# Performance work log

Measured on AMD Instinct MI355X. Metric: run time of the kernel, lower is better.

## Reference

```python
import jax, jax.numpy as jnp
import numpy as np

N_USERS = 50000
N_ITEMS = 100000
N_GROUPS = 20000
D = 128
NNZ_U = 1000000
NNZ_I = 2000000
NNZ_F = 3000000


def setup_inputs() -> dict:
    key = jax.random.key(0)
    ks = jax.random.split(key, 14)
    user_emb = jax.random.normal(ks[0], (N_USERS, D), jnp.float32)
    item_emb = jax.random.normal(ks[1], (N_ITEMS, D), jnp.float32)
    group_emb = jax.random.normal(ks[2], (N_GROUPS, D), jnp.float32)
    # user hypergraph incidence [N_GROUPS, N_USERS] in COO
    u_rows = jax.random.randint(ks[3], (NNZ_U,), 0, N_GROUPS)
    u_cols = jax.random.randint(ks[4], (NNZ_U,), 0, N_USERS)
    u_vals = jax.random.uniform(ks[5], (NNZ_U,), jnp.float32)
    # item hypergraph incidence [N_GROUPS, N_ITEMS] in COO
    i_rows = jax.random.randint(ks[6], (NNZ_I,), 0, N_GROUPS)
    i_cols = jax.random.randint(ks[7], (NNZ_I,), 0, N_ITEMS)
    i_vals = jax.random.uniform(ks[8], (NNZ_I,), jnp.float32)
    # full hypergraph [N_USERS+N_ITEMS, N_GROUPS] in COO
    f_rows = jax.random.randint(ks[9], (NNZ_F,), 0, N_USERS + N_ITEMS)
    f_cols = jax.random.randint(ks[10], (NNZ_F,), 0, N_GROUPS)
    f_vals = jax.random.uniform(ks[11], (NNZ_F,), jnp.float32)
    # nn.Linear(2D, D): weight [D, 2D], bias [D]
    W_agg = jax.random.normal(ks[12], (D, 2 * D), jnp.float32) * 0.05
    b_agg = jnp.zeros((D,), jnp.float32)
    return dict(user_emb=user_emb, item_emb=item_emb, group_emb=group_emb,
                u_rows=u_rows, u_cols=u_cols, u_vals=u_vals,
                i_rows=i_rows, i_cols=i_cols, i_vals=i_vals,
                f_rows=f_rows, f_cols=f_cols, f_vals=f_vals,
                W_agg=W_agg, b_agg=b_agg)


def _spmm(rows, cols, vals, dense, num_rows):
    # sparse[rows, cols]=vals (COO) @ dense -> [num_rows, d]
    return jax.ops.segment_sum(vals[:, None] * dense[cols], rows, num_segments=num_rows)


def reference(user_emb, item_emb, group_emb,
              u_rows, u_cols, u_vals,
              i_rows, i_cols, i_vals,
              f_rows, f_cols, f_vals,
              W_agg, b_agg):
    user_msg = _spmm(u_rows, u_cols, u_vals, user_emb, N_GROUPS)   # [G, D]
    item_msg = _spmm(i_rows, i_cols, i_vals, item_emb, N_GROUPS)   # [G, D]
    msg = jnp.concatenate([user_msg, item_msg], axis=1) @ W_agg.T + b_agg  # [G, D]
    norm_emb = _spmm(f_rows, f_cols, f_vals, msg, N_USERS + N_ITEMS)       # [U+I, D]
    return (norm_emb, msg)
```

## Files before the change

### kernel.cpp

```cpp
#include <hip/hip_runtime.h>
#include <hip/hip_bf16.h>
#include <stdint.h>

#define N_USERS  50000
#define N_ITEMS  100000
#define N_GROUPS 20000
#define DIM      128
#define TWO_DIM  256
#define N_FULL   (N_USERS + N_ITEMS)

#define NBU  625
#define NBI  1250
#define NBF  2344
#define NBT  (NBU + NBI + NBF)
#define CAP  2048

#define TILE_E 32768
#define NT     184
#define NT_PER_XCD 23

__device__ __forceinline__ unsigned bf16_rne(float f)
{
    unsigned u = __float_as_uint(f);
    return (u + 0x7FFFu + ((u >> 16) & 1u)) >> 16;
}
__device__ __forceinline__ unsigned bf16_pack(float a, float b)
{
    return bf16_rne(a) | (bf16_rne(b) << 16);
}

__global__ __launch_bounds__(256) void f32_to_bf16(
    const float4* __restrict__ src, uint2* __restrict__ dst, int n4)
{
    int stride = gridDim.x * 256;
    for (int i = blockIdx.x * 256 + threadIdx.x; i < n4; i += stride) {
        float4 v = src[i];
        dst[i] = make_uint2(bf16_pack(v.x, v.y), bf16_pack(v.z, v.w));
    }
}

__global__ __launch_bounds__(256) void spmm_atomic(
    const int* __restrict__ rows, const int* __restrict__ cols,
    const float* __restrict__ vals, const float* __restrict__ dense,
    float* __restrict__ out, int nnz)
{
    long long t = (long long)blockIdx.x * blockDim.x + threadIdx.x;
    int e    = (int)(t >> 5);
    int lane = (int)(t & 31);
    if (e >= nnz) return;
    int   r = rows[e];
    int   c = cols[e];
    float v = vals[e];
    float4 x = ((const float4*)(dense + (size_t)c * DIM))[lane];
    float* dst = out + (size_t)r * DIM + lane * 4;
    atomicAdd(dst + 0, v * x.x);
    atomicAdd(dst + 1, v * x.y);
    atomicAdd(dst + 2, v * x.z);
    atomicAdd(dst + 3, v * x.w);
}

__device__ __forceinline__ int bucket_of(long long t,
    const int* __restrict__ u_rows, int nnz_u,
    const int* __restrict__ i_rows, int nnz_i,
    const int* __restrict__ f_rows)
{
    if (t < nnz_u)                          return u_rows[t] >> 5;
    else if (t < (long long)nnz_u + nnz_i)  return NBU + (i_rows[t - nnz_u] >> 4);
    else                                    return NBU + NBI + (f_rows[t - nnz_u - nnz_i] >> 6);
}

__global__ __launch_bounds__(512) void hist_tiles(
    const int* __restrict__ u_rows, int nnz_u,
    const int* __restrict__ i_rows, int nnz_i,
    const int* __restrict__ f_rows, int nnz_f,
    unsigned short* __restrict__ M)
{
    __shared__ int h[NBT];
    int tid = threadIdx.x;
    for (int i = tid; i < NBT; i += 512) h[i] = 0;
    __syncthreads();
    int t = (blockIdx.x & 7) * NT_PER_XCD + (blockIdx.x >> 3);
    long long total = (long long)nnz_u + nnz_i + nnz_f;
    long long base  = (long long)t * TILE_E;
    for (int j = tid; j < TILE_E; j += 512) {
        long long e = base + j;
        if (e >= total) break;
        atomicAdd(&h[bucket_of(e, u_rows, nnz_u, i_rows, nnz_i, f_rows)], 1);
    }
    __syncthreads();
    unsigned short* Mrow = M + (size_t)t * NBT;
    for (int i = tid; i < NBT; i += 512) Mrow[i] = (unsigned short)h[i];
}

__global__ __launch_bounds__(64) void tile_prefix(
    unsigned short* __restrict__ M, int* __restrict__ btot)
{
    int b = blockIdx.x * 64 + threadIdx.x;
    if (b >= NBT) return;
    int run = 0;
#pragma unroll 1
    for (int t = 0; t < NT; t += 4) {
        size_t i0 = (size_t)(t + 0) * NBT + b;
        size_t i1 = (size_t)(t + 1) * NBT + b;
        size_t i2 = (size_t)(t + 2) * NBT + b;
        size_t i3 = (size_t)(t + 3) * NBT + b;
        int v0 = M[i0], v1 = M[i1], v2 = M[i2], v3 = M[i3];
        M[i0] = (unsigned short)run; run += v0;
        M[i1] = (unsigned short)run; run += v1;
        M[i2] = (unsigned short)run; run += v2;
        M[i3] = (unsigned short)run; run += v3;
    }
    btot[b] = run;
}

__global__ __launch_bounds__(256) void scan_buckets(
    const int* __restrict__ btot, int* __restrict__ bptr)
{
    __shared__ int wsum[4];
    __shared__ int s_carry;
    int tid = threadIdx.x, lane = tid & 63, wave = tid >> 6;
    if (tid == 0) s_carry = 0;
    __syncthreads();
    for (int base = 0; base < NBT; base += 256) {
        int b = base + tid;
        int x = (b < NBT) ? btot[b] : 0;
        int incl = x;
#pragma unroll
        for (int off = 1; off < 64; off <<= 1) {
            int y = __shfl_up(incl, off, 64);
            if (lane >= off) incl += y;
        }
        if (lane == 63) wsum[wave] = incl;
        __syncthreads();
        int waveOff = 0;
        for (int w = 0; w < wave; ++w) waveOff += wsum[w];
        int carry = s_carry;
        int ex = carry + waveOff + incl - x;
        if (b < NBT) bptr[b] = ex;
        __syncthreads();
        if (tid == 255) s_carry = carry + waveOff + incl;
        __syncthreads();
    }
    if (tid == 0) bptr[NBT] = s_carry;
}

__global__ __launch_bounds__(512) void scatter_tiles(
    const int* __restrict__ u_rows, const int* __restrict__ u_cols,
    const float* __restrict__ u_vals, int nnz_u,
    const int* __restrict__ i_rows, const int* __restrict__ i_cols,
    const float* __restrict__ i_vals, int nnz_i,
    const int* __restrict__ f_rows, const int* __restrict__ f_cols,
    const float* __restrict__ f_vals, int nnz_f,
    const unsigned short* __restrict__ M, const int* __restrict__ bptr,
    uint2* __restrict__ pack)
{
    __shared__ int cur[NBT];
    int tid = threadIdx.x;
    int t = (blockIdx.x & 7) * NT_PER_XCD + (blockIdx.x >> 3);
    const unsigned short* Mrow = M + (size_t)t * NBT;
    for (int i = tid; i < NBT; i += 512) cur[i] = bptr[i] + (int)Mrow[i];
    __syncthreads();
    long long total = (long long)nnz_u + nnz_i + nnz_f;
    long long base  = (long long)t * TILE_E;
    for (int j = tid; j < TILE_E; j += 512) {
        long long e = base + j;
        if (e >= total) break;
        int b, lrow, col; float v;
        if (e < nnz_u) {
            int k = (int)e; int r = u_rows[k];
            b = r >> 5; lrow = r & 31; col = u_cols[k]; v = u_vals[k];
        } else if (e < (long long)nnz_u + nnz_i) {
            int k = (int)(e - nnz_u); int r = i_rows[k];
            b = NBU + (r >> 4); lrow = r & 15; col = i_cols[k]; v = i_vals[k];
        } else {
            int k = (int)(e - nnz_u - nnz_i); int r = f_rows[k];
            b = NBU + NBI + (r >> 6); lrow = r & 63; col = f_cols[k]; v = f_vals[k];
        }
        int p = atomicAdd(&cur[b], 1);
        pack[p] = make_uint2(((unsigned)lrow << 17) | (unsigned)col, __float_as_uint(v));
    }
}

template<bool BF16>
__device__ __forceinline__ void edge_fma(
    const void* __restrict__ dense, unsigned col, int sl, float v, float4& a)
{
    if constexpr (BF16) {
        uint2 q = ((const uint2*)dense)[(size_t)col * 32 + sl];
        float x0 = __uint_as_float(q.x << 16);
        float x1 = __uint_as_float(q.x & 0xFFFF0000u);
        float x2 = __uint_as_float(q.y << 16);
        float x3 = __uint_as_float(q.y & 0xFFFF0000u);
        a.x = fmaf(v, x0, a.x); a.y = fmaf(v, x1, a.y);
        a.z = fmaf(v, x2, a.z); a.w = fmaf(v, x3, a.w);
    } else {
        float4 x = ((const float4*)dense)[(size_t)col * 32 + sl];
        a.x = fmaf(v, x.x, a.x); a.y = fmaf(v, x.y, a.y);
        a.z = fmaf(v, x.z, a.z); a.w = fmaf(v, x.w, a.w);
    }
}

template<bool BF16>
__global__ __launch_bounds__(256) void gather_buckets(
    const int* __restrict__ bptr, const uint2* __restrict__ pack,
    const void* __restrict__ denseA, float* __restrict__ outA,
    int nbA, int rowsA, int nrowsA, int baseA,
    const void* __restrict__ denseB, float* __restrict__ outB,
    int rowsB, int nrowsB, int baseB)
{
    __shared__ uint2 sE[CAP];
    __shared__ int   h[64];
    __shared__ int   o[65];

    const void* dense; float* out; int rowsPB, nrows, lb, bid;
    if ((int)blockIdx.x < nbA) {
        dense = denseA; out = outA; rowsPB = rowsA; nrows = nrowsA;
        lb = blockIdx.x; bid = baseA + lb;
    } else {
        dense = denseB; out = outB; rowsPB = rowsB; nrows = nrowsB;
        lb = blockIdx.x - nbA; bid = baseB + lb;
    }
    int tid = threadIdx.x;
    if (tid < 64) h[tid] = 0;
    __syncthreads();

    int p0 = bptr[bid], p1 = bptr[bid + 1];
    int cnt = p1 - p0;

    for (int j = tid; j < cnt; j += 256)
        atomicAdd(&h[pack[p0 + j].x >> 17], 1);
    __syncthreads();

    if (tid < 64) {
        int x = (tid < rowsPB) ? h[tid] : 0;
        int incl = x;
#pragma unroll
        for (int off = 1; off < 64; off <<= 1) {
            int y = __shfl_up(incl, off, 64);
            if ((tid & 63) >= off) incl += y;
        }
        o[tid + 1] = incl;
        if (tid == 0) o[0] = 0;
        h[tid] = incl - x;
    }
    __syncthreads();

    for (int j = tid; j < cnt; j += 256) {
        uint2 e = pack[p0 + j];
        int r = e.x >> 17;
        int p = atomicAdd(&h[r], 1);
        sE[p] = make_uint2(e.x & 0x1FFFF, e.y);
    }
    __syncthreads();

    int wave = tid >> 6, lane = tid & 63, half = lane >> 5, sl = lane & 31;
    float4* out4 = (float4*)out;
    for (int r = wave; r < rowsPB; r += 4) {
        int s = o[r], epos = o[r + 1];
        float4 a0 = make_float4(0.f, 0.f, 0.f, 0.f);
        float4 a1 = a0, a2 = a0, a3 = a0;
        for (int base = s; base < epos; base += 8) {
            int j0 = base + half, j1 = base + 2 + half;
            int j2 = base + 4 + half, j3 = base + 6 + half;
            if (j0 < epos) {
                uint2 e = sE[j0];
                edge_fma<BF16>(dense, e.x, sl, __uint_as_float(e.y), a0);
            }
            if (j1 < epos) {
                uint2 e = sE[j1];
                edge_fma<BF16>(dense, e.x, sl, __uint_as_float(e.y), a1);
            }
            if (j2 < epos) {
                uint2 e = sE[j2];
                edge_fma<BF16>(dense, e.x, sl, __uint_as_float(e.y), a2);
            }
            if (j3 < epos) {
                uint2 e = sE[j3];
                edge_fma<BF16>(dense, e.x, sl, __uint_as_float(e.y), a3);
            }
        }
        float4 acc;
        acc.x = (a0.x + a1.x) + (a2.x + a3.x);
        acc.y = (a0.y + a1.y) + (a2.y + a3.y);
        acc.z = (a0.z + a1.z) + (a2.z + a3.z);
        acc.w = (a0.w + a1.w) + (a2.w + a3.w);
        acc.x += __shfl_xor(acc.x, 32, 64);
        acc.y += __shfl_xor(acc.y, 32, 64);
        acc.z += __shfl_xor(acc.z, 32, 64);
        acc.w += __shfl_xor(acc.w, 32, 64);
        int row = lb * rowsPB + r;
        if (half == 0 && row < nrows)
            out4[(size_t)row * 32 + sl] = acc;
    }
}

__global__ __launch_bounds__(256) void dense_agg(
    const float* __restrict__ um, const float* __restrict__ im,
    const float* __restrict__ W, const float* __restrict__ b,
    float* __restrict__ msg, uint4* __restrict__ msgb)
{
    __shared__ float As[32][68];
    __shared__ float Ws[64][132];

    int tid = threadIdx.x;
    int tx  = tid & 15;
    int ty  = tid >> 4;
    int rowBase = blockIdx.x * 32;

    float acc[2][8];
#pragma unroll
    for (int i = 0; i < 2; ++i)
#pragma unroll
        for (int j = 0; j < 8; ++j) acc[i][j] = 0.f;

    for (int kc = 0; kc < 4; ++kc) {
        int k0 = kc * 64;
        const float* Asrc = (k0 < DIM) ? um : im;
        int kOff = (k0 < DIM) ? k0 : (k0 - DIM);

#pragma unroll
        for (int l = 0; l < 2; ++l) {
            int idx = tid + l * 256;
            int r   = idx >> 4;
            int kq  = idx & 15;
            int gRow = rowBase + r;
            float4 v = make_float4(0.f, 0.f, 0.f, 0.f);
            if (gRow < N_GROUPS)
                v = *(const float4*)(Asrc + (size_t)gRow * DIM + kOff + kq * 4);
            *(float4*)&As[r][kq * 4] = v;
        }
#pragma unroll
        for (int l = 0; l < 8; ++l) {
            int idx = tid + l * 256;
            int d   = idx >> 4;
            int kq  = idx & 15;
            float4 v = *(const float4*)(W + (size_t)d * TWO_DIM + k0 + kq * 4);
            Ws[kq * 4 + 0][d] = v.x;
            Ws[kq * 4 + 1][d] = v.y;
            Ws[kq * 4 + 2][d] = v.z;
            Ws[kq * 4 + 3][d] = v.w;
        }
        __syncthreads();

        int ty2 = ty * 2;
        int tx8 = tx * 8;
#pragma unroll 8
        for (int k = 0; k < 64; ++k) {
            float a0 = As[ty2 + 0][k];
            float a1 = As[ty2 + 1][k];
            float4 w0 = *(const float4*)&Ws[k][tx8];
            float4 w1 = *(const float4*)&Ws[k][tx8 + 4];
            acc[0][0] = fmaf(a0, w0.x, acc[0][0]);
            acc[0][1] = fmaf(a0, w0.y, acc[0][1]);
            acc[0][2] = fmaf(a0, w0.z, acc[0][2]);
            acc[0][3] = fmaf(a0, w0.w, acc[0][3]);
            acc[0][4] = fmaf(a0, w1.x, acc[0][4]);
            acc[0][5] = fmaf(a0, w1.y, acc[0][5]);
            acc[0][6] = fmaf(a0, w1.z, acc[0][6]);
            acc[0][7] = fmaf(a0, w1.w, acc[0][7]);
            acc[1][0] = fmaf(a1, w0.x, acc[1][0]);
            acc[1][1] = fmaf(a1, w0.y, acc[1][1]);
            acc[1][2] = fmaf(a1, w0.z, acc[1][2]);
            acc[1][3] = fmaf(a1, w0.w, acc[1][3]);
            acc[1][4] = fmaf(a1, w1.x, acc[1][4]);
            acc[1][5] = fmaf(a1, w1.y, acc[1][5]);
            acc[1][6] = fmaf(a1, w1.z, acc[1][6]);
            acc[1][7] = fmaf(a1, w1.w, acc[1][7]);
        }
        __syncthreads();
    }

    int d0 = tx * 8;
    float4 bv0 = *(const float4*)(b + d0);
    float4 bv1 = *(const float4*)(b + d0 + 4);
#pragma unroll
    for (int i = 0; i < 2; ++i) {
        int gRow = rowBase + ty * 2 + i;
        if (gRow < N_GROUPS) {
            float4 o0 = make_float4(acc[i][0] + bv0.x, acc[i][1] + bv0.y,
                                    acc[i][2] + bv0.z, acc[i][3] + bv0.w);
            float4 o1 = make_float4(acc[i][4] + bv1.x, acc[i][5] + bv1.y,
                                    acc[i][6] + bv1.z, acc[i][7] + bv1.w);
            *(float4*)(msg + (size_t)gRow * DIM + d0)     = o0;
            *(float4*)(msg + (size_t)gRow * DIM + d0 + 4) = o1;
            if (msgb) {
                uint4 pb;
                pb.x = bf16_pack(o0.x, o0.y);
                pb.y = bf16_pack(o0.z, o0.w);
                pb.z = bf16_pack(o1.x, o1.y);
                pb.w = bf16_pack(o1.z, o1.w);
                msgb[(size_t)gRow * 16 + tx] = pb;
            }
        }
    }
}

extern "C" void kernel_launch(void* const* d_in, const int* in_sizes, int n_in,
                              void* d_out, int out_size, void* d_ws, size_t ws_size,
                              hipStream_t stream)
{
    const float* user_emb = (const float*)d_in[0];
    const float* item_emb = (const float*)d_in[1];
    const int*   u_rows = (const int*)d_in[3];
    const int*   u_cols = (const int*)d_in[4];
    const float* u_vals = (const float*)d_in[5];
    const int*   i_rows = (const int*)d_in[6];
    const int*   i_cols = (const int*)d_in[7];
    const float* i_vals = (const float*)d_in[8];
    const int*   f_rows = (const int*)d_in[9];
    const int*   f_cols = (const int*)d_in[10];
    const float* f_vals = (const float*)d_in[11];
    const float* W      = (const float*)d_in[12];
    const float* bias   = (const float*)d_in[13];

    int nnz_u = in_sizes[3];
    int nnz_i = in_sizes[6];
    int nnz_f = in_sizes[9];
    long long nnz_tot = (long long)nnz_u + nnz_i + nnz_f;

    float* out  = (float*)d_out;
    float* norm = out;
    float* msg  = out + (size_t)N_FULL * DIM;

    float* um = norm;
    float* im = norm + (size_t)N_GROUPS * DIM;

    auto ceil16 = [](size_t b) { return (b + 15) & ~(size_t)15; };
    size_t need = 0;
    size_t o_M    = need; need += ceil16((size_t)NT * NBT * 2);
    size_t o_btot = need; need += ceil16((size_t)NBT * 4);
    size_t o_bptr = need; need += ceil16((size_t)(NBT + 1) * 4);
    size_t o_pack = need; need += ceil16((size_t)nnz_tot * 8);
    size_t need_base = need;
    size_t o_ebf  = need; need += ceil16((size_t)(N_USERS + N_ITEMS) * DIM * 2);
    size_t o_msgb = need; need += ceil16((size_t)N_GROUPS * DIM * 2);
    size_t need_bf16 = need;

    if (ws_size >= need_base && nnz_tot <= (long long)NT * TILE_E) {
        bool use_bf16 = (ws_size >= need_bf16);
        uint8_t* ws = (uint8_t*)d_ws;
        unsigned short* M = (unsigned short*)(ws + o_M);
        int*   btot = (int*)(ws + o_btot);
        int*   bptr = (int*)(ws + o_bptr);
        uint2* pack = (uint2*)(ws + o_pack);
        uint2* ubf  = (uint2*)(ws + o_ebf);
        uint2* ibf  = ubf + (size_t)N_USERS * 32;
        uint4* msgb = (uint4*)(ws + o_msgb);

        if (use_bf16) {
            f32_to_bf16<<<1024, 256, 0, stream>>>(
                (const float4*)user_emb, ubf, N_USERS * (DIM / 4));
            f32_to_bf16<<<1024, 256, 0, stream>>>(
                (const float4*)item_emb, ibf, N_ITEMS * (DIM / 4));
        }

        hist_tiles<<<NT, 512, 0, stream>>>(
            u_rows, nnz_u, i_rows, nnz_i, f_rows, nnz_f, M);

        tile_prefix<<<(NBT + 63) / 64, 64, 0, stream>>>(M, btot);

        scan_buckets<<<1, 256, 0, stream>>>(btot, bptr);

        scatter_tiles<<<NT, 512, 0, stream>>>(
            u_rows, u_cols, u_vals, nnz_u,
            i_rows, i_cols, i_vals, nnz_i,
            f_rows, f_cols, f_vals, nnz_f,
            M, bptr, pack);

        if (use_bf16) {
            gather_buckets<true><<<NBU + NBI, 256, 0, stream>>>(
                bptr, pack,
                ubf, um, NBU, 32, N_GROUPS, 0,
                ibf, im, 16, N_GROUPS, NBU);

            dense_agg<<<(N_GROUPS + 31) / 32, 256, 0, stream>>>(
                um, im, W, bias, msg, msgb);

            gather_buckets<true><<<NBF, 256, 0, stream>>>(
                bptr, pack,
                msgb, norm, NBF, 64, N_FULL, NBU + NBI,
                msgb, norm, 64, N_FULL, NBU + NBI);
        } else {
            gather_buckets<false><<<NBU + NBI, 256, 0, stream>>>(
                bptr, pack,
                user_emb, um, NBU, 32, N_GROUPS, 0,
                item_emb, im, 16, N_GROUPS, NBU);

            dense_agg<<<(N_GROUPS + 31) / 32, 256, 0, stream>>>(
                um, im, W, bias, msg, nullptr);

            gather_buckets<false><<<NBF, 256, 0, stream>>>(
                bptr, pack,
                msg, norm, NBF, 64, N_FULL, NBU + NBI,
                msg, norm, 64, N_FULL, NBU + NBI);
        }
    } else {
        hipMemsetAsync(norm, 0, (size_t)N_FULL * DIM * sizeof(float), stream);
        auto spmm_blocks = [](int nnz) {
            return (unsigned)(((long long)nnz * 32 + 255) / 256);
        };
        spmm_atomic<<<spmm_blocks(nnz_u), 256, 0, stream>>>(
            u_rows, u_cols, u_vals, user_emb, um, nnz_u);
        spmm_atomic<<<spmm_blocks(nnz_i), 256, 0, stream>>>(
            i_rows, i_cols, i_vals, item_emb, im, nnz_i);
        dense_agg<<<(N_GROUPS + 31) / 32, 256, 0, stream>>>(
            um, im, W, bias, msg, nullptr);
        hipMemsetAsync(norm, 0, (size_t)2 * N_GROUPS * DIM * sizeof(float), stream);
        spmm_atomic<<<spmm_blocks(nnz_f), 256, 0, stream>>>(
            f_rows, f_cols, f_vals, msg, norm, nnz_f);
    }
}
```

Measured before the change: 748.0 us.

## Fuse bf16 conversion into histogram kernel and widen bucket gather to 512 threads

Removes the two standalone f32-to-bf16 conversion launches and runs that conversion as a grid-stride tail inside the histogram kernel. The bucket gather kernel moves to 512 threads (8 waves), stages the packed edges in shared memory once instead of reading them from global memory twice, drops one barrier, and unrolls the per-row edge loop to 8 independent accumulators. It also clamps the bucket count to CAP. The goal is fewer launches, less global traffic and more memory-level parallelism. In exchange, shared memory per block roughly doubles and register pressure rises, which may lower occupancy. The histogram kernel only has 184 blocks, so the fused conversion may run with limited parallelism.

```diff
diff --git a/kernel.cpp b/kernel.cpp
--- a/kernel.cpp
+++ b/kernel.cpp
@@ -27,16 +27,6 @@
 __device__ __forceinline__ unsigned bf16_pack(float a, float b)
 {
     return bf16_rne(a) | (bf16_rne(b) << 16);
-}
-
-__global__ __launch_bounds__(256) void f32_to_bf16(
-    const float4* __restrict__ src, uint2* __restrict__ dst, int n4)
-{
-    int stride = gridDim.x * 256;
-    for (int i = blockIdx.x * 256 + threadIdx.x; i < n4; i += stride) {
-        float4 v = src[i];
-        dst[i] = make_uint2(bf16_pack(v.x, v.y), bf16_pack(v.z, v.w));
-    }
 }
 
 __global__ __launch_bounds__(256) void spmm_atomic(
@@ -73,7 +63,9 @@
     const int* __restrict__ u_rows, int nnz_u,
     const int* __restrict__ i_rows, int nnz_i,
     const int* __restrict__ f_rows, int nnz_f,
-    unsigned short* __restrict__ M)
+    unsigned short* __restrict__ M,
+    const float4* __restrict__ cu_src, uint2* __restrict__ cu_dst, int n4u,
+    const float4* __restrict__ ci_src, uint2* __restrict__ ci_dst, int n4i)
 {
     __shared__ int h[NBT];
     int tid = threadIdx.x;
@@ -90,6 +82,18 @@
     __syncthreads();
     unsigned short* Mrow = M + (size_t)t * NBT;
     for (int i = tid; i < NBT; i += 512) Mrow[i] = (unsigned short)h[i];
+
+    if (cu_dst) {
+        int stride = gridDim.x * 512;
+        for (int i = blockIdx.x * 512 + tid; i < n4u; i += stride) {
+            float4 v = cu_src[i];
+            cu_dst[i] = make_uint2(bf16_pack(v.x, v.y), bf16_pack(v.z, v.w));
+        }
+        for (int i = blockIdx.x * 512 + tid; i < n4i; i += stride) {
+            float4 v = ci_src[i];
+            ci_dst[i] = make_uint2(bf16_pack(v.x, v.y), bf16_pack(v.z, v.w));
+        }
+    }
 }
 
 __global__ __launch_bounds__(64) void tile_prefix(
@@ -201,13 +205,14 @@
 }
 
 template<bool BF16>
-__global__ __launch_bounds__(256) void gather_buckets(
+__global__ __launch_bounds__(512) void gather_buckets(
     const int* __restrict__ bptr, const uint2* __restrict__ pack,
     const void* __restrict__ denseA, float* __restrict__ outA,
     int nbA, int rowsA, int nrowsA, int baseA,
     const void* __restrict__ denseB, float* __restrict__ outB,
     int rowsB, int nrowsB, int baseB)
 {
+    __shared__ uint2 sR[CAP];
     __shared__ uint2 sE[CAP];
     __shared__ int   h[64];
     __shared__ int   o[65];
@@ -222,13 +227,16 @@
     }
     int tid = threadIdx.x;
     if (tid < 64) h[tid] = 0;
-    __syncthreads();
 
     int p0 = bptr[bid], p1 = bptr[bid + 1];
     int cnt = p1 - p0;
-
-    for (int j = tid; j < cnt; j += 256)
-        atomicAdd(&h[pack[p0 + j].x >> 17], 1);
+    if (cnt > CAP) cnt = CAP;
+
+    for (int j = tid; j < cnt; j += 512) sR[j] = pack[p0 + j];
+    __syncthreads();
+
+    for (int j = tid; j < cnt; j += 512)
+        atomicAdd(&h[sR[j].x >> 17], 1);
     __syncthreads();
 
     if (tid < 64) {
@@ -245,8 +253,8 @@
     }
     __syncthreads();
 
-    for (int j = tid; j < cnt; j += 256) {
-        uint2 e = pack[p0 + j];
+    for (int j = tid; j < cnt; j += 512) {
+        uint2 e = sR[j];
         int r = e.x >> 17;
         int p = atomicAdd(&h[r], 1);
         sE[p] = make_uint2(e.x & 0x1FFFF, e.y);
@@ -255,35 +263,29 @@
 
     int wave = tid >> 6, lane = tid & 63, half = lane >> 5, sl = lane & 31;
     float4* out4 = (float4*)out;
-    for (int r = wave; r < rowsPB; r += 4) {
+    for (int r = wave; r < rowsPB; r += 8) {
         int s = o[r], epos = o[r + 1];
         float4 a0 = make_float4(0.f, 0.f, 0.f, 0.f);
-        float4 a1 = a0, a2 = a0, a3 = a0;
-        for (int base = s; base < epos; base += 8) {
-            int j0 = base + half, j1 = base + 2 + half;
-            int j2 = base + 4 + half, j3 = base + 6 + half;
-            if (j0 < epos) {
-                uint2 e = sE[j0];
-                edge_fma<BF16>(dense, e.x, sl, __uint_as_float(e.y), a0);
-            }
-            if (j1 < epos) {
-                uint2 e = sE[j1];
-                edge_fma<BF16>(dense, e.x, sl, __uint_as_float(e.y), a1);
-            }
-            if (j2 < epos) {
-                uint2 e = sE[j2];
-                edge_fma<BF16>(dense, e.x, sl, __uint_as_float(e.y), a2);
-            }
-            if (j3 < epos) {
-                uint2 e = sE[j3];
-                edge_fma<BF16>(dense, e.x, sl, __uint_as_float(e.y), a3);
-            }
+        float4 a1 = a0, a2 = a0, a3 = a0, a4 = a0, a5 = a0, a6 = a0, a7 = a0;
+        for (int base = s; base < epos; base += 16) {
+            int j0 = base +  0 + half, j1 = base +  2 + half;
+            int j2 = base +  4 + half, j3 = base +  6 + half;
+            int j4 = base +  8 + half, j5 = base + 10 + half;
+            int j6 = base + 12 + half, j7 = base + 14 + half;
+            if (j0 < epos) { uint2 e = sE[j0]; edge_fma<BF16>(dense, e.x, sl, __uint_as_float(e.y), a0); }
+            if (j1 < epos) { uint2 e = sE[j1]; edge_fma<BF16>(dense, e.x, sl, __uint_as_float(e.y), a1); }
+            if (j2 < epos) { uint2 e = sE[j2]; edge_fma<BF16>(dense, e.x, sl, __uint_as_float(e.y), a2); }
+            if (j3 < epos) { uint2 e = sE[j3]; edge_fma<BF16>(dense, e.x, sl, __uint_as_float(e.y), a3); }
+            if (j4 < epos) { uint2 e = sE[j4]; edge_fma<BF16>(dense, e.x, sl, __uint_as_float(e.y), a4); }
+            if (j5 < epos) { uint2 e = sE[j5]; edge_fma<BF16>(dense, e.x, sl, __uint_as_float(e.y), a5); }
+            if (j6 < epos) { uint2 e = sE[j6]; edge_fma<BF16>(dense, e.x, sl, __uint_as_float(e.y), a6); }
+            if (j7 < epos) { uint2 e = sE[j7]; edge_fma<BF16>(dense, e.x, sl, __uint_as_float(e.y), a7); }
         }
         float4 acc;
-        acc.x = (a0.x + a1.x) + (a2.x + a3.x);
-        acc.y = (a0.y + a1.y) + (a2.y + a3.y);
-        acc.z = (a0.z + a1.z) + (a2.z + a3.z);
-        acc.w = (a0.w + a1.w) + (a2.w + a3.w);
+        acc.x = ((a0.x + a1.x) + (a2.x + a3.x)) + ((a4.x + a5.x) + (a6.x + a7.x));
+        acc.y = ((a0.y + a1.y) + (a2.y + a3.y)) + ((a4.y + a5.y) + (a6.y + a7.y));
+        acc.z = ((a0.z + a1.z) + (a2.z + a3.z)) + ((a4.z + a5.z) + (a6.z + a7.z));
+        acc.w = ((a0.w + a1.w) + (a2.w + a3.w)) + ((a4.w + a5.w) + (a6.w + a7.w));
         acc.x += __shfl_xor(acc.x, 32, 64);
         acc.y += __shfl_xor(acc.y, 32, 64);
         acc.z += __shfl_xor(acc.z, 32, 64);
@@ -447,15 +449,12 @@
         uint2* ibf  = ubf + (size_t)N_USERS * 32;
         uint4* msgb = (uint4*)(ws + o_msgb);
 
-        if (use_bf16) {
-            f32_to_bf16<<<1024, 256, 0, stream>>>(
-                (const float4*)user_emb, ubf, N_USERS * (DIM / 4));
-            f32_to_bf16<<<1024, 256, 0, stream>>>(
-                (const float4*)item_emb, ibf, N_ITEMS * (DIM / 4));
-        }
-
         hist_tiles<<<NT, 512, 0, stream>>>(
-            u_rows, nnz_u, i_rows, nnz_i, f_rows, nnz_f, M);
+            u_rows, nnz_u, i_rows, nnz_i, f_rows, nnz_f, M,
+            use_bf16 ? (const float4*)user_emb : nullptr,
+            use_bf16 ? ubf : nullptr, N_USERS * (DIM / 4),
+            use_bf16 ? (const float4*)item_emb : nullptr,
+            use_bf16 ? ibf : nullptr, N_ITEMS * (DIM / 4));
 
         tile_prefix<<<(NBT + 63) / 64, 64, 0, stream>>>(M, btot);
 
@@ -468,7 +467,7 @@
             M, bptr, pack);
 
         if (use_bf16) {
-            gather_buckets<true><<<NBU + NBI, 256, 0, stream>>>(
+            gather_buckets<true><<<NBU + NBI, 512, 0, stream>>>(
                 bptr, pack,
                 ubf, um, NBU, 32, N_GROUPS, 0,
                 ibf, im, 16, N_GROUPS, NBU);
@@ -476,12 +475,12 @@
             dense_agg<<<(N_GROUPS + 31) / 32, 256, 0, stream>>>(
                 um, im, W, bias, msg, msgb);
 
-            gather_buckets<true><<<NBF, 256, 0, stream>>>(
+            gather_buckets<true><<<NBF, 512, 0, stream>>>(
                 bptr, pack,
                 msgb, norm, NBF, 64, N_FULL, NBU + NBI,
                 msgb, norm, 64, N_FULL, NBU + NBI);
         } else {
-            gather_buckets<false><<<NBU + NBI, 256, 0, stream>>>(
+            gather_buckets<false><<<NBU + NBI, 512, 0, stream>>>(
                 bptr, pack,
                 user_emb, um, NBU, 32, N_GROUPS, 0,
                 item_emb, im, 16, N_GROUPS, NBU);
@@ -489,7 +488,7 @@
             dense_agg<<<(N_GROUPS + 31) / 32, 256, 0, stream>>>(
                 um, im, W, bias, msg, nullptr);
 
-            gather_buckets<false><<<NBF, 256, 0, stream>>>(
+            gather_buckets<false><<<NBF, 512, 0, stream>>>(
                 bptr, pack,
                 msg, norm, NBF, 64, N_FULL, NBU + NBI,
                 msg, norm, 64, N_FULL, NBU + NBI);
```

Result: faster. 728.7 us (-2.6%).
